# Performance work log

Measured on AMD Instinct MI355X. Metric: run time of the kernel, lower is better.

## Reference

```python
import jax, jax.numpy as jnp
import numpy as np

N_NODES = 100000
N_EDGES = 1600000
D = 128          # in = hidden = out channels
N_LAYERS = 3


def setup_inputs() -> dict:
    key = jax.random.key(0)
    ks = jax.random.split(key, 20)
    inp = {
        "x": jax.random.normal(ks[0], (N_NODES, D), jnp.float32),
        "edge_index": jax.random.randint(ks[1], (2, N_EDGES), 0, N_NODES, dtype=jnp.int64),
    }
    s = 1.0 / np.sqrt(D)
    k = 2
    for l in range(N_LAYERS):
        inp[f"w1_{l}"] = jax.random.normal(ks[k], (D, D), jnp.float32) * s; k += 1
        inp[f"b1_{l}"] = jnp.zeros((D,), jnp.float32)
        inp[f"w2_{l}"] = jax.random.normal(ks[k], (D, D), jnp.float32) * s; k += 1
        inp[f"b2_{l}"] = jnp.zeros((D,), jnp.float32)
    # JK concat: 3 layers * D channels -> out D
    inp["jk_w"] = jax.random.normal(ks[k], (N_LAYERS * D, D), jnp.float32) * (1.0 / np.sqrt(N_LAYERS * D))
    inp["jk_b"] = jnp.zeros((D,), jnp.float32)
    return inp


def _gin_layer(x, src, dst, w1, b1, w2, b2):
    # GINConv, eps=0: h = (1+eps)*x + sum_{j in N(i)} x_j ; then MLP Lin-ReLU-Lin
    agg = jax.ops.segment_sum(x[src], dst, num_segments=N_NODES)  # [N, D]
    h = x + agg
    h = jax.nn.relu(h @ w1 + b1)
    return h @ w2 + b2


def reference(x, edge_index, w1_0, b1_0, w2_0, b2_0, w1_1, b1_1, w2_1, b2_1,
              w1_2, b1_2, w2_2, b2_2, jk_w, jk_b):
    src, dst = edge_index[0], edge_index[1]
    layers = [(w1_0, b1_0, w2_0, b2_0), (w1_1, b1_1, w2_1, b2_1), (w1_2, b1_2, w2_2, b2_2)]
    xs = []
    for i, (w1, b1, w2, b2) in enumerate(layers):
        # dropout is identity in eval mode
        residual = x  # skip_proj is Identity since in==out channels
        x = _gin_layer(x, src, dst, w1, b1, w2, b2) + residual
        if i != N_LAYERS - 1:
            x = jax.nn.elu(x)
        xs.append(x)
    x = jnp.concatenate(xs, axis=-1)  # JK 'cat' -> [N, 3*D]
    return x @ jk_w + jk_b
```

## Files before the change

kernel.cpp:

```cpp
#include <hip/hip_runtime.h>

typedef __bf16 bf16x8 __attribute__((ext_vector_type(8)));
typedef float f32x4 __attribute__((ext_vector_type(4)));

#define CHUNK 4096
#define NBUCK 512

struct WPack { const float* p[9]; };

__device__ inline __bf16 f2bf(float f){ return (__bf16)f; }

__device__ inline int hswz(int r, int c){
  return (r << 7) + ((((c >> 3) ^ (r & 7)) << 3) | (c & 7));
}
__device__ inline const __bf16* hvec(const __bf16* H, int r, int g){
  return H + (r << 7) + (((g ^ (r & 7)) & 15) << 3);
}

__global__ __launch_bounds__(256) void prep_kernel(WPack pk, __bf16* __restrict__ wf,
    const float* __restrict__ x, __bf16* __restrict__ xb, int n8){
  int b = blockIdx.x, t = threadIdx.x;
  if (b < 576){
    int tid = b*256 + t;
    int m = tid >> 14;
    int r = tid & 16383;
    int j = r & 7;
    int lane = (r >> 3) & 63;
    int ks = (r >> 9) & 3;
    int c = r >> 11;
    int k = ks*32 + ((lane>>4)<<3) + j;
    int col = (c<<4) + (lane & 15);
    wf[tid] = f2bf(pk.p[m][k*128 + col]);
  } else {
    int i = (b - 576)*256 + t;
    if (i >= n8) return;
    f32x4 a = ((const f32x4*)x)[2*i];
    f32x4 bb = ((const f32x4*)x)[2*i+1];
    bf16x8 r;
    r[0]=f2bf(a[0]); r[1]=f2bf(a[1]); r[2]=f2bf(a[2]); r[3]=f2bf(a[3]);
    r[4]=f2bf(bb[0]); r[5]=f2bf(bb[1]); r[6]=f2bf(bb[2]); r[7]=f2bf(bb[3]);
    ((bf16x8*)xb)[i] = r;
  }
}

__global__ __launch_bounds__(256) void p1_count(const int* __restrict__ ei, int E, int NBLK,
    int* __restrict__ cnt){
  __shared__ int h[NBUCK];
  int b = blockIdx.x, t = threadIdx.x;
  h[t] = 0; h[t + 256] = 0;
  __syncthreads();
  int base = b*CHUNK;
  int lim = E - base; if (lim > CHUNK) lim = CHUNK;
  for (int i = t; i < lim; i += 256)
    atomicAdd(&h[ei[E + base + i] >> 8], 1);
  __syncthreads();
  cnt[t*NBLK + b] = h[t];
  cnt[(t + 256)*NBLK + b] = h[t + 256];
}

__global__ __launch_bounds__(256) void scan1_kernel(const int* __restrict__ cnt, int* __restrict__ bsum, int L){
  __shared__ int sh[256];
  int b = blockIdx.x, t = threadIdx.x;
  int base = b*2048 + t*8;
  int s = 0;
  #pragma unroll
  for (int j = 0; j < 8; j++){ int i = base + j; if (i < L) s += cnt[i]; }
  sh[t] = s; __syncthreads();
  for (int off = 128; off > 0; off >>= 1){
    if (t < off) sh[t] += sh[t + off];
    __syncthreads();
  }
  if (t == 0) bsum[b] = sh[0];
}

__global__ __launch_bounds__(256) void scan2_kernel(const int* __restrict__ bsum, int* __restrict__ boff,
                                                    int NB, int* __restrict__ total_out){
  __shared__ int sh[256];
  int t = threadIdx.x;
  int v = (t < NB) ? bsum[t] : 0;
  sh[t] = v; __syncthreads();
  for (int off = 1; off < 256; off <<= 1){
    int u = (t >= off) ? sh[t - off] : 0;
    __syncthreads();
    sh[t] += u;
    __syncthreads();
  }
  if (t < NB) boff[t] = sh[t] - v;
  if (t == 255) *total_out = sh[255];
}

__global__ __launch_bounds__(256) void scan3_kernel(const int* __restrict__ cnt, const int* __restrict__ boff,
                                                    int* __restrict__ off, int L){
  __shared__ int sh[256];
  int b = blockIdx.x, t = threadIdx.x;
  int base = b*2048 + t*8;
  int loc[8]; int s = 0;
  #pragma unroll
  for (int j = 0; j < 8; j++){ int i = base + j; int d = (i < L) ? cnt[i] : 0; loc[j] = d; s += d; }
  sh[t] = s; __syncthreads();
  for (int o = 1; o < 256; o <<= 1){
    int u = (t >= o) ? sh[t - o] : 0;
    __syncthreads();
    sh[t] += u;
    __syncthreads();
  }
  int excl = boff[b] + sh[t] - s;
  #pragma unroll
  for (int j = 0; j < 8; j++){ int i = base + j; if (i < L) off[i] = excl; excl += loc[j]; }
}

__global__ __launch_bounds__(256) void p3_scatter(const int* __restrict__ ei, int E, int NBLK,
    const int* __restrict__ off, int* __restrict__ tpack){
  __shared__ int cur[NBUCK];
  int b = blockIdx.x, t = threadIdx.x;
  cur[t]       = off[t*NBLK + b];
  cur[t + 256] = off[(t + 256)*NBLK + b];
  __syncthreads();
  int base = b*CHUNK;
  int lim = E - base; if (lim > CHUNK) lim = CHUNK;
  for (int i = t; i < lim; i += 256){
    int s = ei[base + i];
    int d = ei[E + base + i];
    int p = atomicAdd(&cur[d >> 8], 1);
    tpack[p] = (s << 8) | (d & 255);
  }
}

__global__ __launch_bounds__(256) void p4_build(const int* __restrict__ tpack,
    const int* __restrict__ off, int NBLK, int E, int N,
    int* __restrict__ rs, int* __restrict__ csr){
  __shared__ int dc[256], sc[256];
  int q = blockIdx.x, t = threadIdx.x;
  int bstart = off[q*NBLK];
  int bend = (q == NBUCK-1) ? E : off[(q+1)*NBLK];
  dc[t] = 0;
  __syncthreads();
  for (int i = bstart + t; i < bend; i += 256)
    atomicAdd(&dc[tpack[i] & 255], 1);
  __syncthreads();
  int v = dc[t];
  sc[t] = v; __syncthreads();
  for (int o = 1; o < 256; o <<= 1){
    int u = (t >= o) ? sc[t - o] : 0;
    __syncthreads();
    sc[t] += u;
    __syncthreads();
  }
  int ex = sc[t] - v;
  int gd = q*256 + t;
  if (gd < N) rs[gd] = bstart + ex;
  __syncthreads();
  dc[t] = ex;
  __syncthreads();
  for (int i = bstart + t; i < bend; i += 256){
    int p = tpack[i];
    int r = atomicAdd(&dc[p & 255], 1);
    csr[bstart + r] = p >> 8;
  }
}

__global__ __launch_bounds__(256) void agg_kernel(const __bf16* __restrict__ xb,
    const int* __restrict__ rs, const int* __restrict__ csr,
    __bf16* __restrict__ hb, int N)
{
  int node = blockIdx.x*4 + (threadIdx.x >> 6);
  if (node >= N) return;
  int lane = threadIdx.x & 63;
  int quad = lane >> 4;
  int l16  = lane & 15;
  int s = rs[node], e = rs[node+1];
  float a[8] = {0.f,0.f,0.f,0.f,0.f,0.f,0.f,0.f};
  for (int base = s; base < e; base += 64){
    int idx = base + lane;
    int nb = (idx < e) ? csr[idx] : 0;
    int cnt = e - base; if (cnt > 64) cnt = 64;
    int t = 0;
    #pragma unroll 2
    for (; t + 8 <= cnt; t += 8){
      int sA = __shfl(nb, t + quad);
      int sB = __shfl(nb, t + 4 + quad);
      bf16x8 vA = ((const bf16x8*)(xb + (long)sA*128))[l16];
      bf16x8 vB = ((const bf16x8*)(xb + (long)sB*128))[l16];
      #pragma unroll
      for (int j = 0; j < 8; j++) a[j] += (float)vA[j] + (float)vB[j];
    }
    for (; t < cnt; t += 4){
      int i = t + quad;
      int ic = (i < cnt) ? i : (cnt - 1);
      int sA = __shfl(nb, ic);
      bf16x8 vA = ((const bf16x8*)(xb + (long)sA*128))[l16];
      if (i < cnt){
        #pragma unroll
        for (int j = 0; j < 8; j++) a[j] += (float)vA[j];
      }
    }
  }
  if (quad == 0){
    bf16x8 sv = ((const bf16x8*)(xb + (long)node*128))[l16];
    #pragma unroll
    for (int j = 0; j < 8; j++) a[j] += (float)sv[j];
  }
  #pragma unroll
  for (int j = 0; j < 8; j++){
    a[j] += __shfl_xor(a[j], 16);
    a[j] += __shfl_xor(a[j], 32);
  }
  if (quad == 0){
    bf16x8 r;
    #pragma unroll
    for (int j = 0; j < 8; j++) r[j] = f2bf(a[j]);
    ((bf16x8*)(hb + (long)node*128))[l16] = r;
  }
}

template<int ACT2>
__global__ __launch_bounds__(256, 4) void fused_mlp(const __bf16* __restrict__ A,
    const __bf16* __restrict__ wf1, const __bf16* __restrict__ wf2,
    const float* __restrict__ b1, const float* __restrict__ b2,
    const __bf16* __restrict__ res, __bf16* __restrict__ out, int M)
{
  __shared__ __bf16 H[64*128];
  int lane = threadIdx.x & 63;
  int wid = threadIdx.x >> 6;
  int quad = lane >> 4;
  long row0 = (long)blockIdx.x * 64;
  const bf16x8* w1v = (const bf16x8*)wf1;
  const bf16x8* w2v = (const bf16x8*)wf2;
  bf16x8 bv1[2][4], bv2[2][4];
  #pragma unroll
  for (int c2 = 0; c2 < 2; c2++)
    #pragma unroll
    for (int ks = 0; ks < 4; ks++){
      bv1[c2][ks] = w1v[((wid*2 + c2)*4 + ks)*64 + lane];
      bv2[c2][ks] = w2v[((wid*2 + c2)*4 + ks)*64 + lane];
    }
  int col0 = wid*32 + (lane & 15);
  float bb1_0 = b1[col0], bb1_1 = b1[col0 + 16];
  float bb2_0 = b2[col0], bb2_1 = b2[col0 + 16];
  int koff = quad << 3;
  #pragma unroll 2
  for (int rt = 0; rt < 4; rt++){
    long row = row0 + rt*16 + (lane & 15);
    long rowc = (row < M) ? row : (long)(M-1);
    const __bf16* ap = A + rowc*128 + koff;
    bf16x8 av[4];
    #pragma unroll
    for (int ks = 0; ks < 4; ks++)
      av[ks] = *(const bf16x8*)(ap + ks*32);
    f32x4 acc0 = {0.f,0.f,0.f,0.f}, acc1 = {0.f,0.f,0.f,0.f};
    #pragma unroll
    for (int ks = 0; ks < 4; ks++){
      acc0 = __builtin_amdgcn_mfma_f32_16x16x32_bf16(av[ks], bv1[0][ks], acc0, 0, 0, 0);
      acc1 = __builtin_amdgcn_mfma_f32_16x16x32_bf16(av[ks], bv1[1][ks], acc1, 0, 0, 0);
    }
    int r0 = rt*16 + (quad << 2);
    #pragma unroll
    for (int c2 = 0; c2 < 2; c2++){
      f32x4 acc = c2 ? acc1 : acc0;
      int col = col0 + c2*16;
      float bb = c2 ? bb1_1 : bb1_0;
      #pragma unroll
      for (int i = 0; i < 4; i++)
        H[hswz(r0 + i, col)] = f2bf(fmaxf(acc[i] + bb, 0.f));
    }
  }
  __syncthreads();
  #pragma unroll 2
  for (int rt = 0; rt < 4; rt++){
    float rv[2][4];
    #pragma unroll
    for (int c2 = 0; c2 < 2; c2++)
      #pragma unroll
      for (int i = 0; i < 4; i++){
        long orow = row0 + rt*16 + (quad << 2) + i;
        rv[c2][i] = (orow < M) ? (float)res[orow*128 + col0 + c2*16] : 0.f;
      }
    int r = rt*16 + (lane & 15);
    bf16x8 av[4];
    #pragma unroll
    for (int ks = 0; ks < 4; ks++)
      av[ks] = *(const bf16x8*)hvec(H, r, 4*ks + quad);
    f32x4 acc0 = {0.f,0.f,0.f,0.f}, acc1 = {0.f,0.f,0.f,0.f};
    #pragma unroll
    for (int ks = 0; ks < 4; ks++){
      acc0 = __builtin_amdgcn_mfma_f32_16x16x32_bf16(av[ks], bv2[0][ks], acc0, 0, 0, 0);
      acc1 = __builtin_amdgcn_mfma_f32_16x16x32_bf16(av[ks], bv2[1][ks], acc1, 0, 0, 0);
    }
    long orow0 = row0 + rt*16 + (quad << 2);
    #pragma unroll
    for (int c2 = 0; c2 < 2; c2++){
      f32x4 acc = c2 ? acc1 : acc0;
      int col = col0 + c2*16;
      float bb = c2 ? bb2_1 : bb2_0;
      #pragma unroll
      for (int i = 0; i < 4; i++){
        long orow = orow0 + i;
        if (orow < M){
          float v = acc[i] + bb + rv[c2][i];
          if (ACT2 == 2) v = (v > 0.f) ? v : (__expf(v) - 1.f);
          out[orow*128 + col] = f2bf(v);
        }
      }
    }
  }
}

__global__ __launch_bounds__(256, 4) void fused_mlp_jk(const __bf16* __restrict__ A,
    const __bf16* __restrict__ y1g, const __bf16* __restrict__ y2g,
    const __bf16* __restrict__ wf1, const __bf16* __restrict__ wf2,
    const __bf16* __restrict__ wfjk,
    const float* __restrict__ b1, const float* __restrict__ b2,
    const float* __restrict__ jkb, float* __restrict__ out, int M)
{
  __shared__ __bf16 H[64*128];
  __shared__ __bf16 Y2L[64*128];
  int lane = threadIdx.x & 63;
  int wid = threadIdx.x >> 6;
  int quad = lane >> 4;
  long row0 = (long)blockIdx.x * 64;
  const bf16x8* w1v = (const bf16x8*)wf1;
  const bf16x8* w2v = (const bf16x8*)wf2;
  bf16x8 bv1[2][4], bv2[2][4];
  #pragma unroll
  for (int c2 = 0; c2 < 2; c2++)
    #pragma unroll
    for (int ks = 0; ks < 4; ks++){
      bv1[c2][ks] = w1v[((wid*2 + c2)*4 + ks)*64 + lane];
      bv2[c2][ks] = w2v[((wid*2 + c2)*4 + ks)*64 + lane];
    }
  int col0 = wid*32 + (lane & 15);
  float bb1_0 = b1[col0], bb1_1 = b1[col0 + 16];
  float bb2_0 = b2[col0], bb2_1 = b2[col0 + 16];
  int koff = quad << 3;
  #pragma unroll 2
  for (int rt = 0; rt < 4; rt++){
    long row = row0 + rt*16 + (lane & 15);
    long rowc = (row < M) ? row : (long)(M-1);
    const __bf16* ap = A + rowc*128 + koff;
    bf16x8 av[4];
    #pragma unroll
    for (int ks = 0; ks < 4; ks++)
      av[ks] = *(const bf16x8*)(ap + ks*32);
    f32x4 acc0 = {0.f,0.f,0.f,0.f}, acc1 = {0.f,0.f,0.f,0.f};
    #pragma unroll
    for (int ks = 0; ks < 4; ks++){
      acc0 = __builtin_amdgcn_mfma_f32_16x16x32_bf16(av[ks], bv1[0][ks], acc0, 0, 0, 0);
      acc1 = __builtin_amdgcn_mfma_f32_16x16x32_bf16(av[ks], bv1[1][ks], acc1, 0, 0, 0);
    }
    int r0 = rt*16 + (quad << 2);
    #pragma unroll
    for (int c2 = 0; c2 < 2; c2++){
      f32x4 acc = c2 ? acc1 : acc0;
      int col = col0 + c2*16;
      float bb = c2 ? bb1_1 : bb1_0;
      #pragma unroll
      for (int i = 0; i < 4; i++)
        H[hswz(r0 + i, col)] = f2bf(fmaxf(acc[i] + bb, 0.f));
    }
  }
  __syncthreads();
  #pragma unroll 1
  for (int rt = 0; rt < 4; rt++){
    int r = rt*16 + (lane & 15);
    bf16x8 av[4];
    #pragma unroll
    for (int ks = 0; ks < 4; ks++)
      av[ks] = *(const bf16x8*)hvec(H, r, 4*ks + quad);
    f32x4 acc0 = {0.f,0.f,0.f,0.f}, acc1 = {0.f,0.f,0.f,0.f};
    #pragma unroll
    for (int ks = 0; ks < 4; ks++){
      acc0 = __builtin_amdgcn_mfma_f32_16x16x32_bf16(av[ks], bv2[0][ks], acc0, 0, 0, 0);
      acc1 = __builtin_amdgcn_mfma_f32_16x16x32_bf16(av[ks], bv2[1][ks], acc1, 0, 0, 0);
    }
    long orow0 = row0 + rt*16 + (quad << 2);
    int r0 = rt*16 + (quad << 2);
    __bf16 rb[2][4];
    #pragma unroll
    for (int c2 = 0; c2 < 2; c2++)
      #pragma unroll
      for (int i = 0; i < 4; i++){
        long orow = orow0 + i;
        rb[c2][i] = (orow < M) ? y2g[orow*128 + col0 + c2*16] : f2bf(0.f);
      }
    __syncthreads();
    #pragma unroll
    for (int c2 = 0; c2 < 2; c2++){
      f32x4 acc = c2 ? acc1 : acc0;
      int col = col0 + c2*16;
      float bb = c2 ? bb2_1 : bb2_0;
      #pragma unroll
      for (int i = 0; i < 4; i++){
        Y2L[hswz(r0 + i, col)] = rb[c2][i];
        H[hswz(r0 + i, col)] = f2bf(acc[i] + bb + (float)rb[c2][i]);
      }
    }
  }
  __syncthreads();
  const bf16x8* wjv = (const bf16x8*)wfjk;
  float jb0 = jkb[col0], jb1 = jkb[col0 + 16];
  f32x4 acc[4][2];
  #pragma unroll
  for (int q = 0; q < 4; q++){
    acc[q][0] = (f32x4){jb0, jb0, jb0, jb0};
    acc[q][1] = (f32x4){jb1, jb1, jb1, jb1};
  }
  {
    bf16x8 bv[2][4];
    #pragma unroll
    for (int c2 = 0; c2 < 2; c2++)
      #pragma unroll
      for (int ks = 0; ks < 4; ks++)
        bv[c2][ks] = wjv[(size_t)((wid*2 + c2)*4 + ks)*64 + lane];
    #pragma unroll
    for (int q = 0; q < 4; q++){
      long row = row0 + q*16 + (lane & 15);
      long rowc = (row < M) ? row : (long)(M-1);
      const __bf16* ap = y1g + rowc*128 + koff;
      bf16x8 av[4];
      #pragma unroll
      for (int ks = 0; ks < 4; ks++)
        av[ks] = *(const bf16x8*)(ap + ks*32);
      #pragma unroll
      for (int ks = 0; ks < 4; ks++){
        acc[q][0] = __builtin_amdgcn_mfma_f32_16x16x32_bf16(av[ks], bv[0][ks], acc[q][0], 0, 0, 0);
        acc[q][1] = __builtin_amdgcn_mfma_f32_16x16x32_bf16(av[ks], bv[1][ks], acc[q][1], 0, 0, 0);
      }
    }
  }
  #pragma unroll 1
  for (int src = 1; src < 3; src++){
    const __bf16* Hs = (src == 1) ? Y2L : H;
    bf16x8 bv[2][4];
    #pragma unroll
    for (int c2 = 0; c2 < 2; c2++)
      #pragma unroll
      for (int ks = 0; ks < 4; ks++)
        bv[c2][ks] = wjv[(size_t)src*2048 + (size_t)((wid*2 + c2)*4 + ks)*64 + lane];
    #pragma unroll
    for (int q = 0; q < 4; q++){
      int r = q*16 + (lane & 15);
      bf16x8 av[4];
      #pragma unroll
      for (int ks = 0; ks < 4; ks++)
        av[ks] = *(const bf16x8*)hvec(Hs, r, 4*ks + quad);
      #pragma unroll
      for (int ks = 0; ks < 4; ks++){
        acc[q][0] = __builtin_amdgcn_mfma_f32_16x16x32_bf16(av[ks], bv[0][ks], acc[q][0], 0, 0, 0);
        acc[q][1] = __builtin_amdgcn_mfma_f32_16x16x32_bf16(av[ks], bv[1][ks], acc[q][1], 0, 0, 0);
      }
    }
  }
  #pragma unroll
  for (int q = 0; q < 4; q++){
    long orow0 = row0 + q*16 + (quad << 2);
    #pragma unroll
    for (int c2 = 0; c2 < 2; c2++){
      int col = col0 + c2*16;
      #pragma unroll
      for (int i = 0; i < 4; i++){
        long orow = orow0 + i;
        if (orow < M)
          out[orow*128 + col] = acc[q][c2][i];
      }
    }
  }
}

extern "C" void kernel_launch(void* const* d_in, const int* in_sizes, int n_in,
                              void* d_out, int out_size, void* d_ws, size_t ws_size,
                              hipStream_t stream)
{
  const float* x   = (const float*)d_in[0];
  const int*   ei  = (const int*)d_in[1];
  const float* w1[3] = {(const float*)d_in[2], (const float*)d_in[6], (const float*)d_in[10]};
  const float* b1[3] = {(const float*)d_in[3], (const float*)d_in[7], (const float*)d_in[11]};
  const float* w2[3] = {(const float*)d_in[4], (const float*)d_in[8], (const float*)d_in[12]};
  const float* b2[3] = {(const float*)d_in[5], (const float*)d_in[9], (const float*)d_in[13]};
  const float* jkw = (const float*)d_in[14];
  const float* jkb = (const float*)d_in[15];
  int N = in_sizes[0] / 128;
  int E = in_sizes[1] / 2;
  float* outp = (float*)d_out;

  char* wptr = (char*)d_ws;
  auto alloc = [&](size_t bytes)->void*{
    void* p = (void*)wptr; wptr += (bytes + 255) & ~(size_t)255; return p;
  };
  int NBLK = (E + CHUNK - 1) / CHUNK;
  int L = NBUCK * NBLK;
  int* rs    = (int*)alloc((size_t)(N+1)*4);
  int* csr   = (int*)alloc((size_t)E*4);
  int* tpack = (int*)alloc((size_t)E*4);
  int* cnt   = (int*)alloc((size_t)L*4);
  int* off   = (int*)alloc((size_t)L*4);
  __bf16* y[3];
  for (int i = 0; i < 3; i++) y[i] = (__bf16*)alloc((size_t)N*128*2);
  __bf16* hb = (__bf16*)alloc((size_t)N*128*2);
  __bf16* wf = (__bf16*)alloc((size_t)9*16384*2);
  int nsb = (L + 2047) / 2048;
  int* bsum = (int*)alloc((size_t)nsb*4);
  int* boff = (int*)alloc((size_t)nsb*4);

  WPack pk;
  pk.p[0] = w1[0]; pk.p[1] = w2[0];
  pk.p[2] = w1[1]; pk.p[3] = w2[1];
  pk.p[4] = w1[2]; pk.p[5] = w2[2];
  pk.p[6] = jkw; pk.p[7] = jkw + 16384; pk.p[8] = jkw + 32768;
  int n8 = N*128/8;
  prep_kernel<<<576 + (n8 + 255)/256, 256, 0, stream>>>(pk, wf, x, y[0], n8);

  p1_count<<<NBLK, 256, 0, stream>>>(ei, E, NBLK, cnt);
  scan1_kernel<<<nsb, 256, 0, stream>>>(cnt, bsum, L);
  scan2_kernel<<<1, 256, 0, stream>>>(bsum, boff, nsb, rs + N);
  scan3_kernel<<<nsb, 256, 0, stream>>>(cnt, boff, off, L);
  p3_scatter<<<NBLK, 256, 0, stream>>>(ei, E, NBLK, off, tpack);
  p4_build<<<NBUCK, 256, 0, stream>>>(tpack, off, NBLK, E, N, rs, csr);

  int gemm_blocks = (N + 63)/64;
  for (int l = 0; l < 3; l++){
    agg_kernel<<<(N + 3)/4, 256, 0, stream>>>(y[l], rs, csr, hb, N);
    if (l < 2)
      fused_mlp<2><<<gemm_blocks, 256, 0, stream>>>(hb, wf + (size_t)(2*l)*16384, wf + (size_t)(2*l+1)*16384,
                                                    b1[l], b2[l], y[l], y[l+1], N);
    else
      fused_mlp_jk<<<gemm_blocks, 256, 0, stream>>>(hb, y[1], y[2],
                                                    wf + (size_t)4*16384, wf + (size_t)5*16384, wf + (size_t)6*16384,
                                                    b1[2], b2[2], jkb, outp, N);
  }
}
```

Before: 358.4 us.

## Prefetch y2 tile into LDS up front and reorder JK GEMM to hide loads

The final fused MLP+JK kernel now loads the y2 residual tile into LDS with coalesced 16-byte vector loads at kernel start, replacing scalar per-element global loads issued inside the second GEMM loop. The second GEMM now computes all four row tiles into registers before a single barrier and the epilogue, replacing a per-iteration barrier. The JK stage prefetches part of the y1 global operand before running the LDS-sourced products, so those global loads overlap with MFMA work. The cost is higher register pressure from the held accumulators and prefetched operands, which could reduce occupancy at launch bounds of 4 blocks.

After: 370.6 us. +3.4%, slower.

```diff
diff --git a/kernel.cpp b/kernel.cpp
--- a/kernel.cpp
+++ b/kernel.cpp
@@ -318,6 +318,15 @@
   int wid = threadIdx.x >> 6;
   int quad = lane >> 4;
   long row0 = (long)blockIdx.x * 64;
+  #pragma unroll
+  for (int k = 0; k < 4; k++){
+    int flat = (int)threadIdx.x + 256*k;
+    int r = flat >> 4, gg = flat & 15;
+    long row = row0 + r;
+    long rowc = (row < M) ? row : (long)(M-1);
+    bf16x8 v = *(const bf16x8*)(y2g + rowc*128 + gg*8);
+    *(bf16x8*)(Y2L + (r << 7) + (((gg ^ (r & 7)) & 15) << 3)) = v;
+  }
   const bf16x8* w1v = (const bf16x8*)wf1;
   const bf16x8* w2v = (const bf16x8*)wf2;
   bf16x8 bv1[2][4], bv2[2][4];
@@ -359,39 +368,34 @@
     }
   }
   __syncthreads();
-  #pragma unroll 1
+  f32x4 acc2[4][2];
+  #pragma unroll
   for (int rt = 0; rt < 4; rt++){
     int r = rt*16 + (lane & 15);
     bf16x8 av[4];
     #pragma unroll
     for (int ks = 0; ks < 4; ks++)
       av[ks] = *(const bf16x8*)hvec(H, r, 4*ks + quad);
-    f32x4 acc0 = {0.f,0.f,0.f,0.f}, acc1 = {0.f,0.f,0.f,0.f};
+    acc2[rt][0] = (f32x4){0.f,0.f,0.f,0.f};
+    acc2[rt][1] = (f32x4){0.f,0.f,0.f,0.f};
     #pragma unroll
     for (int ks = 0; ks < 4; ks++){
-      acc0 = __builtin_amdgcn_mfma_f32_16x16x32_bf16(av[ks], bv2[0][ks], acc0, 0, 0, 0);
-      acc1 = __builtin_amdgcn_mfma_f32_16x16x32_bf16(av[ks], bv2[1][ks], acc1, 0, 0, 0);
-    }
-    long orow0 = row0 + rt*16 + (quad << 2);
+      acc2[rt][0] = __builtin_amdgcn_mfma_f32_16x16x32_bf16(av[ks], bv2[0][ks], acc2[rt][0], 0, 0, 0);
+      acc2[rt][1] = __builtin_amdgcn_mfma_f32_16x16x32_bf16(av[ks], bv2[1][ks], acc2[rt][1], 0, 0, 0);
+    }
+  }
+  __syncthreads();
+  #pragma unroll
+  for (int rt = 0; rt < 4; rt++){
     int r0 = rt*16 + (quad << 2);
-    __bf16 rb[2][4];
-    #pragma unroll
-    for (int c2 = 0; c2 < 2; c2++)
-      #pragma unroll
-      for (int i = 0; i < 4; i++){
-        long orow = orow0 + i;
-        rb[c2][i] = (orow < M) ? y2g[orow*128 + col0 + c2*16] : f2bf(0.f);
-      }
-    __syncthreads();
     #pragma unroll
     for (int c2 = 0; c2 < 2; c2++){
-      f32x4 acc = c2 ? acc1 : acc0;
       int col = col0 + c2*16;
       float bb = c2 ? bb2_1 : bb2_0;
       #pragma unroll
       for (int i = 0; i < 4; i++){
-        Y2L[hswz(r0 + i, col)] = rb[c2][i];
-        H[hswz(r0 + i, col)] = f2bf(acc[i] + bb + (float)rb[c2][i]);
+        int idx = hswz(r0 + i, col);
+        H[idx] = f2bf(acc2[rt][c2][i] + bb + (float)Y2L[idx]);
       }
     }
   }
@@ -404,6 +408,39 @@
     acc[q][0] = (f32x4){jb0, jb0, jb0, jb0};
     acc[q][1] = (f32x4){jb1, jb1, jb1, jb1};
   }
+  bf16x8 av1[2][4];
+  #pragma unroll
+  for (int q = 0; q < 2; q++){
+    long row = row0 + q*16 + (lane & 15);
+    long rowc = (row < M) ? row : (long)(M-1);
+    const __bf16* ap = y1g + rowc*128 + koff;
+    #pragma unroll
+    for (int ks = 0; ks < 4; ks++)
+      av1[q][ks] = *(const bf16x8*)(ap + ks*32);
+  }
+  #pragma unroll 1
+  for (int src = 1; src < 3; src++){
+    const __bf16* Hs = (src == 1) ? Y2L : H;
+    bf16x8 bv[2][4];
+    #pragma unroll
+    for (int c2 = 0; c2 < 2; c2++)
+      #pragma unroll
+      for (int ks = 0; ks < 4; ks++)
+        bv[c2][ks] = wjv[(size_t)src*2048 + (size_t)((wid*2 + c2)*4 + ks)*64 + lane];
+    #pragma unroll
+    for (int q = 0; q < 4; q++){
+      int r = q*16 + (lane & 15);
+      bf16x8 av[4];
+      #pragma unroll
+      for (int ks = 0; ks < 4; ks++)
+        av[ks] = *(const bf16x8*)hvec(Hs, r, 4*ks + quad);
+      #pragma unroll
+      for (int ks = 0; ks < 4; ks++){
+        acc[q][0] = __builtin_amdgcn_mfma_f32_16x16x32_bf16(av[ks], bv[0][ks], acc[q][0], 0, 0, 0);
+        acc[q][1] = __builtin_amdgcn_mfma_f32_16x16x32_bf16(av[ks], bv[1][ks], acc[q][1], 0, 0, 0);
+      }
+    }
+  }
   {
     bf16x8 bv[2][4];
     #pragma unroll
@@ -412,7 +449,14 @@
       for (int ks = 0; ks < 4; ks++)
         bv[c2][ks] = wjv[(size_t)((wid*2 + c2)*4 + ks)*64 + lane];
     #pragma unroll
-    for (int q = 0; q < 4; q++){
+    for (int q = 0; q < 2; q++)
+      #pragma unroll
+      for (int ks = 0; ks < 4; ks++){
+        acc[q][0] = __builtin_amdgcn_mfma_f32_16x16x32_bf16(av1[q][ks], bv[0][ks], acc[q][0], 0, 0, 0);
+        acc[q][1] = __builtin_amdgcn_mfma_f32_16x16x32_bf16(av1[q][ks], bv[1][ks], acc[q][1], 0, 0, 0);
+      }
+    #pragma unroll
+    for (int q = 2; q < 4; q++){
       long row = row0 + q*16 + (lane & 15);
       long rowc = (row < M) ? row : (long)(M-1);
       const __bf16* ap = y1g + rowc*128 + koff;
@@ -420,29 +464,6 @@
       #pragma unroll
       for (int ks = 0; ks < 4; ks++)
         av[ks] = *(const bf16x8*)(ap + ks*32);
-      #pragma unroll
-      for (int ks = 0; ks < 4; ks++){
-        acc[q][0] = __builtin_amdgcn_mfma_f32_16x16x32_bf16(av[ks], bv[0][ks], acc[q][0], 0, 0, 0);
-        acc[q][1] = __builtin_amdgcn_mfma_f32_16x16x32_bf16(av[ks], bv[1][ks], acc[q][1], 0, 0, 0);
-      }
-    }
-  }
-  #pragma unroll 1
-  for (int src = 1; src < 3; src++){
-    const __bf16* Hs = (src == 1) ? Y2L : H;
-    bf16x8 bv[2][4];
-    #pragma unroll
-    for (int c2 = 0; c2 < 2; c2++)
-      #pragma unroll
-      for (int ks = 0; ks < 4; ks++)
-        bv[c2][ks] = wjv[(size_t)src*2048 + (size_t)((wid*2 + c2)*4 + ks)*64 + lane];
-    #pragma unroll
-    for (int q = 0; q < 4; q++){
-      int r = q*16 + (lane & 15);
-      bf16x8 av[4];
-      #pragma unroll
-      for (int ks = 0; ks < 4; ks++)
-        av[ks] = *(const bf16x8*)hvec(Hs, r, 4*ks + quad);
       #pragma unroll
       for (int ks = 0; ks < 4; ks++){
         acc[q][0] = __builtin_amdgcn_mfma_f32_16x16x32_bf16(av[ks], bv[0][ks], acc[q][0], 0, 0, 0);
```
